# Performance work log

Hardware: AMD Instinct MI355X
Metric: run time of the kernel (lower is better)

Reference implementation:

```python
import jax, jax.numpy as jnp
import numpy as np

INPUT_DIM = 1024
OUTPUT_DIM = 1024
DEGREE = 8
N_TOKENS = 8192


def setup_inputs() -> dict:
    key = jax.random.key(0)
    k1, k2 = jax.random.split(key)
    x = jax.random.normal(k1, (N_TOKENS, INPUT_DIM), dtype=jnp.float32)
    # xavier_normal_ with gain = 1/(input_dim*(degree+1)) over fan dims (output_dim, degree+1)
    fan_in, fan_out = OUTPUT_DIM, DEGREE + 1  # torch treats dim0/dim1 as fans; scale is tiny anyway
    gain = 1.0 / (INPUT_DIM * (DEGREE + 1))
    std = gain * np.sqrt(2.0 / (INPUT_DIM + OUTPUT_DIM))
    cheby_coeffs = std * jax.random.normal(k2, (INPUT_DIM, OUTPUT_DIM, DEGREE + 1), dtype=jnp.float32)
    return {"x": x, "cheby_coeffs": cheby_coeffs}


def reference(x, cheby_coeffs):
    # x: (..., input_dim) -> y: (..., output_dim)
    degree_p1 = cheby_coeffs.shape[-1]
    theta = jnp.arccos(jnp.tanh(x))                      # (..., i)
    arange = jnp.arange(degree_p1, dtype=x.dtype)        # (d,)
    basis = jnp.cos(theta[..., None] * arange)           # (..., i, d) Chebyshev T_d(tanh(x))
    y = jnp.einsum('...id,iod->...o', basis, cheby_coeffs)
    return y
```

## Files before the change

### kernel.cpp

```cpp
#include <hip/hip_runtime.h>


typedef __bf16 bf16;
typedef __bf16 bf16x8 __attribute__((ext_vector_type(8)));
typedef float f32x2 __attribute__((ext_vector_type(2)));
typedef float f32x4 __attribute__((ext_vector_type(4)));
typedef float f32x16 __attribute__((ext_vector_type(16)));

__device__ __forceinline__ void g2lds16(const void* g, void* l) {
  __builtin_amdgcn_global_load_lds(
      (const __attribute__((address_space(1))) unsigned int*)g,
      (__attribute__((address_space(3))) unsigned int*)l, 16, 0, 0);
}

__device__ __forceinline__ float fast_tanh(float a) {
  float e = __expf(a + a);
  return 1.f - 2.f * __builtin_amdgcn_rcpf(e + 1.f);
}

__global__ __launch_bounds__(256)
void cheby_prep(const float* __restrict__ x, const float* __restrict__ C,
                bf16* __restrict__ Bt, float* __restrict__ bias_p,
                float* __restrict__ th) {
  const int bid = blockIdx.x, tid = threadIdx.x;
  if (bid >= 1024) {
    const int r = bid - 1024;
    f32x4 v = *(const f32x4*)(x + (size_t)r * 1024 + tid * 4);
    f32x4 t;
    #pragma unroll
    for (int j = 0; j < 4; ++j) t[j] = fast_tanh(v[j]);
    *(f32x2*)(th + (size_t)r * 1024 + tid * 2)       = (f32x2){t.x, t.z};
    *(f32x2*)(th + (size_t)r * 1024 + 512 + tid * 2) = (f32x2){t.y, t.w};
    return;
  }
  __shared__ float tile[32][292];
  const int i0 = (bid >> 5) * 32, o0 = (bid & 31) * 32;
  {
    const int r = tid >> 3, seg = tid & 7;
    const float* src = C + (size_t)(i0 + r) * 9216 + (size_t)o0 * 9 + seg * 36;
    float* dst = &tile[r][seg * 36];
    #pragma unroll
    for (int v = 0; v < 9; ++v) *(f32x4*)(dst + v * 4) = *(const f32x4*)(src + v * 4);
  }
  __syncthreads();
  #pragma unroll
  for (int j = 0; j < 4; ++j) {
    int e = tid + 256 * j;
    int il = e >> 5, ol = e & 31;
    int i = i0 + il, o = o0 + ol;
    bf16x8 v;
    #pragma unroll
    for (int d = 0; d < 8; ++d) v[d] = (bf16)tile[il][ol * 9 + 1 + d];
    size_t idx16 = ((size_t)((o >> 7) * 128 + (i >> 3)) * 8 + (i & 7)) * 128 + (o & 127);
    *(bf16x8*)&Bt[idx16 * 8] = v;
  }
  if (tid < 32) {
    float s = 0.f;
    #pragma unroll
    for (int i = 0; i < 32; ++i) s += tile[i][tid * 9];
    bias_p[(size_t)(bid >> 5) * 1024 + o0 + tid] = s;
  }
}

__global__ __launch_bounds__(256, 2)
void cheby_gemm(const float* __restrict__ th, const bf16* __restrict__ Bt,
                const float* __restrict__ bias_p, float* __restrict__ out) {
  __shared__ bf16 Bs[2][8192];

  const int tid  = threadIdx.x;
  const int lane = tid & 63, w = tid >> 6;
  const int wm = w >> 1, wn = w & 1;
  const int nb = blockIdx.x & 7, mb = blockIdx.x >> 3;
  const int t0 = mb * 128, o0 = nb * 128;
  const int ml = lane & 31, h = lane >> 5;

  const float* xr0 = th + (size_t)(t0 + wm * 64 + ml) * 1024 + h * 512;
  const float* xr1 = xr0 + 32 * 1024;
  const bf16* btw = Bt + ((size_t)nb * 128 * 1024 + (size_t)w * 256 + lane) * 8;

  f32x16 acc[2][2];
  #pragma unroll
  for (int a = 0; a < 2; ++a)
    #pragma unroll
    for (int b = 0; b < 2; ++b)
      #pragma unroll
      for (int r = 0; r < 16; ++r) acc[a][b][r] = 0.f;

  bf16x8 afrA[2][4], afrB[2][4];
  f32x4 xv0, xv1;

  auto gen = [&](bf16x8 (&dst)[2][4], f32x4 s0, f32x4 s1) {
    #pragma unroll
    for (int ks = 0; ks < 4; ++ks) {
      f32x2 t  = {s0[ks], s1[ks]};
      f32x2 t2 = t + t;
      f32x2 prev = {1.f, 1.f}, cur = t;
      #pragma unroll
      for (int j = 0; j < 8; ++j) {
        dst[0][ks][j] = (bf16)cur.x;
        dst[1][ks][j] = (bf16)cur.y;
        f32x2 nx = t2 * cur - prev;
        prev = cur; cur = nx;
      }
    }
  };

  {
    f32x4 s0 = *(const f32x4*)(xr0), s1 = *(const f32x4*)(xr1);
    gen(afrA, s0, s1);
    xv0 = *(const f32x4*)(xr0 + 4);
    xv1 = *(const f32x4*)(xr1 + 4);
  }
  #pragma unroll
  for (int b = 0; b < 4; ++b)
    g2lds16(btw + (size_t)b * 64 * 8, &Bs[0][(w * 256 + b * 64) * 8]);

  auto stage = [&](int s, int bi, bf16x8 (&cur)[2][4], bf16x8 (&nxt)[2][4]) {
    __syncthreads();
    if (s < 127) {
      const bf16* g = btw + (size_t)(s + 1) * 8192;
      #pragma unroll
      for (int b = 0; b < 4; ++b)
        g2lds16(g + (size_t)b * 64 * 8, &Bs[bi ^ 1][(w * 256 + b * 64) * 8]);
    }
    bf16x8 bfr[4][2];
    #pragma unroll
    for (int ks = 0; ks < 4; ++ks) {
      const int ce = ((ks * 2 + h) * 128 + wn * 64 + ml) * 8;
      bfr[ks][0] = *(const bf16x8*)&Bs[bi][ce];
      bfr[ks][1] = *(const bf16x8*)&Bs[bi][ce + 32 * 8];
    }
    if (s < 127) {
      gen(nxt, xv0, xv1);
      if (s < 126) {
        xv0 = *(const f32x4*)(xr0 + (s + 2) * 4);
        xv1 = *(const f32x4*)(xr1 + (s + 2) * 4);
      }
    }
    #pragma unroll
    for (int ks = 0; ks < 4; ++ks) {
      acc[0][0] = __builtin_amdgcn_mfma_f32_32x32x16_bf16(cur[0][ks], bfr[ks][0], acc[0][0], 0, 0, 0);
      acc[0][1] = __builtin_amdgcn_mfma_f32_32x32x16_bf16(cur[0][ks], bfr[ks][1], acc[0][1], 0, 0, 0);
      acc[1][0] = __builtin_amdgcn_mfma_f32_32x32x16_bf16(cur[1][ks], bfr[ks][0], acc[1][0], 0, 0, 0);
      acc[1][1] = __builtin_amdgcn_mfma_f32_32x32x16_bf16(cur[1][ks], bfr[ks][1], acc[1][1], 0, 0, 0);
    }
  };

  #pragma unroll 1
  for (int s2 = 0; s2 < 64; ++s2) {
    stage(2 * s2,     0, afrA, afrB);
    stage(2 * s2 + 1, 1, afrB, afrA);
  }

  const int c0 = o0 + wn * 64 + ml;
  float bv0 = 0.f, bv1 = 0.f;
  #pragma unroll
  for (int p = 0; p < 32; ++p) {
    bv0 += bias_p[(size_t)p * 1024 + c0];
    bv1 += bias_p[(size_t)p * 1024 + c0 + 32];
  }
  #pragma unroll
  for (int mt = 0; mt < 2; ++mt)
    #pragma unroll
    for (int r = 0; r < 16; ++r) {
      int row = t0 + wm * 64 + mt * 32 + (r & 3) + 8 * (r >> 2) + 4 * h;
      float* po = out + (size_t)row * 1024 + c0;
      po[0]  = acc[mt][0][r] + bv0;
      po[32] = acc[mt][1][r] + bv1;
    }
}

__global__ __launch_bounds__(256)
void cheby_naive(const float* __restrict__ x, const float* __restrict__ C,
                 float* __restrict__ out) {
  const int t = blockIdx.x, tid = threadIdx.x;
  float acc[4] = {0.f, 0.f, 0.f, 0.f};
  for (int i = 0; i < 1024; ++i) {
    float th = tanhf(x[(size_t)t * 1024 + i]);
    float T[9]; T[0] = 1.f; T[1] = th;
    #pragma unroll
    for (int d = 2; d < 9; ++d) T[d] = 2.f * th * T[d - 1] - T[d - 2];
    #pragma unroll
    for (int j = 0; j < 4; ++j) {
      const float* cp = &C[((size_t)i * 1024 + tid + j * 256) * 9];
      float s = 0.f;
      #pragma unroll
      for (int d = 0; d < 9; ++d) s += T[d] * cp[d];
      acc[j] += s;
    }
  }
  #pragma unroll
  for (int j = 0; j < 4; ++j) out[(size_t)t * 1024 + tid + j * 256] = acc[j];
}

extern "C" void kernel_launch(void* const* d_in, const int* in_sizes, int n_in,
                              void* d_out, int out_size, void* d_ws, size_t ws_size,
                              hipStream_t stream) {
  (void)in_sizes; (void)n_in; (void)out_size;
  const float* x = (const float*)d_in[0];
  const float* C = (const float*)d_in[1];
  float* out = (float*)d_out;

  const size_t bt_bytes = (size_t)8 * 128 * 1024 * 8 * sizeof(bf16);
  const size_t bp_bytes = (size_t)32 * 1024 * sizeof(float);
  const size_t th_bytes = (size_t)8192 * 1024 * sizeof(float);

  if (ws_size >= bt_bytes + bp_bytes + th_bytes) {
    bf16*  Bt     = (bf16*)d_ws;
    float* bias_p = (float*)((char*)d_ws + bt_bytes);
    float* th     = (float*)((char*)d_ws + bt_bytes + bp_bytes);
    cheby_prep<<<9216, 256, 0, stream>>>(x, C, Bt, bias_p, th);
    cheby_gemm<<<512, 256, 0, stream>>>(th, Bt, bias_p, out);
  } else {
    cheby_naive<<<8192, 256, 0, stream>>>(x, C, out);
  }
}
```

Before: 269.2 us.

## Split GEMM K dimension in two with atomic accumulation into zeroed output

```diff
diff --git a/kernel.cpp b/kernel.cpp
--- a/kernel.cpp
+++ b/kernel.cpp
@@ -21,7 +21,7 @@
 __global__ __launch_bounds__(256)
 void cheby_prep(const float* __restrict__ x, const float* __restrict__ C,
                 bf16* __restrict__ Bt, float* __restrict__ bias_p,
-                float* __restrict__ th) {
+                float* __restrict__ th, float* __restrict__ out) {
   const int bid = blockIdx.x, tid = threadIdx.x;
   if (bid >= 1024) {
     const int r = bid - 1024;
@@ -31,6 +31,7 @@
     for (int j = 0; j < 4; ++j) t[j] = fast_tanh(v[j]);
     *(f32x2*)(th + (size_t)r * 1024 + tid * 2)       = (f32x2){t.x, t.z};
     *(f32x2*)(th + (size_t)r * 1024 + 512 + tid * 2) = (f32x2){t.y, t.w};
+    *(f32x4*)(out + (size_t)r * 1024 + tid * 4) = (f32x4){0.f, 0.f, 0.f, 0.f};
     return;
   }
   __shared__ float tile[32][292];
@@ -62,7 +63,7 @@
   }
 }
 
-__global__ __launch_bounds__(256, 2)
+__global__ __launch_bounds__(256, 4)
 void cheby_gemm(const float* __restrict__ th, const bf16* __restrict__ Bt,
                 const float* __restrict__ bias_p, float* __restrict__ out) {
   __shared__ bf16 Bs[2][8192];
@@ -70,7 +71,9 @@
   const int tid  = threadIdx.x;
   const int lane = tid & 63, w = tid >> 6;
   const int wm = w >> 1, wn = w & 1;
-  const int nb = blockIdx.x & 7, mb = blockIdx.x >> 3;
+  const int nb = blockIdx.x & 7;
+  const int kh = (blockIdx.x >> 3) & 1;
+  const int mb = blockIdx.x >> 4;
   const int t0 = mb * 128, o0 = nb * 128;
   const int ml = lane & 31, h = lane >> 5;
 
@@ -78,6 +81,8 @@
   const float* xr1 = xr0 + 32 * 1024;
   const bf16* btw = Bt + ((size_t)nb * 128 * 1024 + (size_t)w * 256 + lane) * 8;
 
+  const int sbeg = kh * 64, send = sbeg + 64;
+
   f32x16 acc[2][2];
   #pragma unroll
   for (int a = 0; a < 2; ++a)
@@ -86,78 +91,66 @@
       #pragma unroll
       for (int r = 0; r < 16; ++r) acc[a][b][r] = 0.f;
 
-  bf16x8 afrA[2][4], afrB[2][4];
-  f32x4 xv0, xv1;
-
-  auto gen = [&](bf16x8 (&dst)[2][4], f32x4 s0, f32x4 s1) {
+  f32x4 xv0 = *(const f32x4*)(xr0 + sbeg * 4);
+  f32x4 xv1 = *(const f32x4*)(xr1 + sbeg * 4);
+
+  #pragma unroll
+  for (int b = 0; b < 4; ++b)
+    g2lds16(btw + (size_t)sbeg * 8192 + (size_t)b * 64 * 8,
+            &Bs[0][(w * 256 + b * 64) * 8]);
+
+  #pragma unroll 1
+  for (int s = sbeg; s < send; ++s) {
+    const int bi = (s - sbeg) & 1;
+    __syncthreads();
+    if (s < send - 1) {
+      const bf16* g = btw + (size_t)(s + 1) * 8192;
+      #pragma unroll
+      for (int b = 0; b < 4; ++b)
+        g2lds16(g + (size_t)b * 64 * 8, &Bs[bi ^ 1][(w * 256 + b * 64) * 8]);
+    }
+
+    f32x4 sd0 = xv0, sd1 = xv1;
+    if (s < send - 1) {
+      xv0 = *(const f32x4*)(xr0 + (s + 1) * 4);
+      xv1 = *(const f32x4*)(xr1 + (s + 1) * 4);
+    }
+
+    bf16x8 afr[2][4];
     #pragma unroll
     for (int ks = 0; ks < 4; ++ks) {
-      f32x2 t  = {s0[ks], s1[ks]};
+      f32x2 t  = {sd0[ks], sd1[ks]};
       f32x2 t2 = t + t;
       f32x2 prev = {1.f, 1.f}, cur = t;
       #pragma unroll
       for (int j = 0; j < 8; ++j) {
-        dst[0][ks][j] = (bf16)cur.x;
-        dst[1][ks][j] = (bf16)cur.y;
+        afr[0][ks][j] = (bf16)cur.x;
+        afr[1][ks][j] = (bf16)cur.y;
         f32x2 nx = t2 * cur - prev;
         prev = cur; cur = nx;
       }
     }
-  };
-
-  {
-    f32x4 s0 = *(const f32x4*)(xr0), s1 = *(const f32x4*)(xr1);
-    gen(afrA, s0, s1);
-    xv0 = *(const f32x4*)(xr0 + 4);
-    xv1 = *(const f32x4*)(xr1 + 4);
-  }
-  #pragma unroll
-  for (int b = 0; b < 4; ++b)
-    g2lds16(btw + (size_t)b * 64 * 8, &Bs[0][(w * 256 + b * 64) * 8]);
-
-  auto stage = [&](int s, int bi, bf16x8 (&cur)[2][4], bf16x8 (&nxt)[2][4]) {
-    __syncthreads();
-    if (s < 127) {
-      const bf16* g = btw + (size_t)(s + 1) * 8192;
-      #pragma unroll
-      for (int b = 0; b < 4; ++b)
-        g2lds16(g + (size_t)b * 64 * 8, &Bs[bi ^ 1][(w * 256 + b * 64) * 8]);
-    }
-    bf16x8 bfr[4][2];
+
     #pragma unroll
     for (int ks = 0; ks < 4; ++ks) {
       const int ce = ((ks * 2 + h) * 128 + wn * 64 + ml) * 8;
-      bfr[ks][0] = *(const bf16x8*)&Bs[bi][ce];
-      bfr[ks][1] = *(const bf16x8*)&Bs[bi][ce + 32 * 8];
-    }
-    if (s < 127) {
-      gen(nxt, xv0, xv1);
-      if (s < 126) {
-        xv0 = *(const f32x4*)(xr0 + (s + 2) * 4);
-        xv1 = *(const f32x4*)(xr1 + (s + 2) * 4);
-      }
-    }
-    #pragma unroll
-    for (int ks = 0; ks < 4; ++ks) {
-      acc[0][0] = __builtin_amdgcn_mfma_f32_32x32x16_bf16(cur[0][ks], bfr[ks][0], acc[0][0], 0, 0, 0);
-      acc[0][1] = __builtin_amdgcn_mfma_f32_32x32x16_bf16(cur[0][ks], bfr[ks][1], acc[0][1], 0, 0, 0);
-      acc[1][0] = __builtin_amdgcn_mfma_f32_32x32x16_bf16(cur[1][ks], bfr[ks][0], acc[1][0], 0, 0, 0);
-      acc[1][1] = __builtin_amdgcn_mfma_f32_32x32x16_bf16(cur[1][ks], bfr[ks][1], acc[1][1], 0, 0, 0);
-    }
-  };
-
-  #pragma unroll 1
-  for (int s2 = 0; s2 < 64; ++s2) {
-    stage(2 * s2,     0, afrA, afrB);
-    stage(2 * s2 + 1, 1, afrB, afrA);
+      bf16x8 b0 = *(const bf16x8*)&Bs[bi][ce];
+      bf16x8 b1 = *(const bf16x8*)&Bs[bi][ce + 32 * 8];
+      acc[0][0] = __builtin_amdgcn_mfma_f32_32x32x16_bf16(afr[0][ks], b0, acc[0][0], 0, 0, 0);
+      acc[0][1] = __builtin_amdgcn_mfma_f32_32x32x16_bf16(afr[0][ks], b1, acc[0][1], 0, 0, 0);
+      acc[1][0] = __builtin_amdgcn_mfma_f32_32x32x16_bf16(afr[1][ks], b0, acc[1][0], 0, 0, 0);
+      acc[1][1] = __builtin_amdgcn_mfma_f32_32x32x16_bf16(afr[1][ks], b1, acc[1][1], 0, 0, 0);
+    }
   }
 
   const int c0 = o0 + wn * 64 + ml;
   float bv0 = 0.f, bv1 = 0.f;
-  #pragma unroll
-  for (int p = 0; p < 32; ++p) {
-    bv0 += bias_p[(size_t)p * 1024 + c0];
-    bv1 += bias_p[(size_t)p * 1024 + c0 + 32];
+  if (kh == 0) {
+    #pragma unroll
+    for (int p = 0; p < 32; ++p) {
+      bv0 += bias_p[(size_t)p * 1024 + c0];
+      bv1 += bias_p[(size_t)p * 1024 + c0 + 32];
+    }
   }
   #pragma unroll
   for (int mt = 0; mt < 2; ++mt)
@@ -165,8 +158,8 @@
     for (int r = 0; r < 16; ++r) {
       int row = t0 + wm * 64 + mt * 32 + (r & 3) + 8 * (r >> 2) + 4 * h;
       float* po = out + (size_t)row * 1024 + c0;
-      po[0]  = acc[mt][0][r] + bv0;
-      po[32] = acc[mt][1][r] + bv1;
+      unsafeAtomicAdd(&po[0],  acc[mt][0][r] + bv0);
+      unsafeAtomicAdd(&po[32], acc[mt][1][r] + bv1);
     }
 }
 
@@ -209,8 +202,8 @@
     bf16*  Bt     = (bf16*)d_ws;
     float* bias_p = (float*)((char*)d_ws + bt_bytes);
     float* th     = (float*)((char*)d_ws + bt_bytes + bp_bytes);
-    cheby_prep<<<9216, 256, 0, stream>>>(x, C, Bt, bias_p, th);
-    cheby_gemm<<<512, 256, 0, stream>>>(th, Bt, bias_p, out);
+    cheby_prep<<<9216, 256, 0, stream>>>(x, C, Bt, bias_p, th, out);
+    cheby_gemm<<<1024, 256, 0, stream>>>(th, Bt, bias_p, out);
   } else {
     cheby_naive<<<8192, 256, 0, stream>>>(x, C, out);
   }
```

New measurement: 299.3 us. 1.11x slower.

## Load B fragments directly from global into registers, dropping LDS staging and barriers

Applied to the files above, without the earlier changes.

```diff
diff --git a/kernel.cpp b/kernel.cpp
--- a/kernel.cpp
+++ b/kernel.cpp
@@ -6,12 +6,6 @@
 typedef float f32x2 __attribute__((ext_vector_type(2)));
 typedef float f32x4 __attribute__((ext_vector_type(4)));
 typedef float f32x16 __attribute__((ext_vector_type(16)));
-
-__device__ __forceinline__ void g2lds16(const void* g, void* l) {
-  __builtin_amdgcn_global_load_lds(
-      (const __attribute__((address_space(1))) unsigned int*)g,
-      (__attribute__((address_space(3))) unsigned int*)l, 16, 0, 0);
-}
 
 __device__ __forceinline__ float fast_tanh(float a) {
   float e = __expf(a + a);
@@ -65,18 +59,18 @@
 __global__ __launch_bounds__(256, 2)
 void cheby_gemm(const float* __restrict__ th, const bf16* __restrict__ Bt,
                 const float* __restrict__ bias_p, float* __restrict__ out) {
-  __shared__ bf16 Bs[2][8192];
-
   const int tid  = threadIdx.x;
   const int lane = tid & 63, w = tid >> 6;
-  const int wm = w >> 1, wn = w & 1;
-  const int nb = blockIdx.x & 7, mb = blockIdx.x >> 3;
-  const int t0 = mb * 128, o0 = nb * 128;
   const int ml = lane & 31, h = lane >> 5;
-
-  const float* xr0 = th + (size_t)(t0 + wm * 64 + ml) * 1024 + h * 512;
-  const float* xr1 = xr0 + 32 * 1024;
-  const bf16* btw = Bt + ((size_t)nb * 128 * 1024 + (size_t)w * 256 + lane) * 8;
+  const int nb = blockIdx.x & 7;
+  const int mb = blockIdx.x >> 3;
+  const int wn = w & 1, wm = w >> 1;
+  const int t0 = mb * 128 + wm * 64;
+  const int o0 = nb * 128 + wn * 64;
+
+  const bf16* btl = Bt + (((size_t)nb * 1024 + h) * 128 + (size_t)wn * 64 + ml) * 8;
+  const float* sp0 = th + (size_t)(t0 + ml) * 1024 + h * 512;
+  const float* sp1 = sp0 + 32 * 1024;
 
   f32x16 acc[2][2];
   #pragma unroll
@@ -86,85 +80,79 @@
       #pragma unroll
       for (int r = 0; r < 16; ++r) acc[a][b][r] = 0.f;
 
-  bf16x8 afrA[2][4], afrB[2][4];
-  f32x4 xv0, xv1;
-
-  auto gen = [&](bf16x8 (&dst)[2][4], f32x4 s0, f32x4 s1) {
-    #pragma unroll
-    for (int ks = 0; ks < 4; ++ks) {
-      f32x2 t  = {s0[ks], s1[ks]};
-      f32x2 t2 = t + t;
-      f32x2 prev = {1.f, 1.f}, cur = t;
-      #pragma unroll
-      for (int j = 0; j < 8; ++j) {
-        dst[0][ks][j] = (bf16)cur.x;
-        dst[1][ks][j] = (bf16)cur.y;
-        f32x2 nx = t2 * cur - prev;
-        prev = cur; cur = nx;
+  f32x4  sa[4], sb[4];
+  bf16x8 bfr[2][4][2];
+
+  sa[0] = *(const f32x4*)(sp0);     sb[0] = *(const f32x4*)(sp1);
+  sa[1] = *(const f32x4*)(sp0 + 4); sb[1] = *(const f32x4*)(sp1 + 4);
+  #pragma unroll
+  for (int ks = 0; ks < 4; ++ks) {
+    bfr[0][ks][0] = *(const bf16x8*)(btl + ks * 2048);
+    bfr[0][ks][1] = *(const bf16x8*)(btl + ks * 2048 + 256);
+  }
+
+  #pragma unroll 1
+  for (int s4 = 0; s4 < 128; s4 += 4) {
+    #pragma unroll
+    for (int u = 0; u < 4; ++u) {
+      const int s = s4 + u;
+      {
+        int sl = s + 2; if (sl > 127) sl = 127;
+        sa[(u + 2) & 3] = *(const f32x4*)(sp0 + sl * 4);
+        sb[(u + 2) & 3] = *(const f32x4*)(sp1 + sl * 4);
+      }
+      {
+        int bl = s + 1; if (bl > 127) bl = 127;
+        const bf16* g = btl + (size_t)bl * 8192;
+        #pragma unroll
+        for (int ks = 0; ks < 4; ++ks) {
+          bfr[(u + 1) & 1][ks][0] = *(const bf16x8*)(g + ks * 2048);
+          bfr[(u + 1) & 1][ks][1] = *(const bf16x8*)(g + ks * 2048 + 256);
+        }
+      }
+      bf16x8 afr[2][4];
+      #pragma unroll
+      for (int r = 0; r < 2; ++r) {
+        const f32x4 sd = r ? sb[u & 3] : sa[u & 3];
+        #pragma unroll
+        for (int ks = 0; ks < 4; ++ks) {
+          const float t  = sd[ks];
+          const float T2 = __builtin_fmaf(t + t, t, -1.f);
+          const float c2 = T2 + T2;
+          const f32x2 c2v = {c2, c2};
+          f32x2 pm1 = {t, 1.f};
+          f32x2 p   = {t, T2};
+          #pragma unroll
+          for (int j2 = 0; j2 < 4; ++j2) {
+            afr[r][ks][2 * j2]     = (bf16)p.x;
+            afr[r][ks][2 * j2 + 1] = (bf16)p.y;
+            f32x2 pn = c2v * p - pm1;
+            pm1 = p; p = pn;
+          }
+        }
+      }
+      #pragma unroll
+      for (int ks = 0; ks < 4; ++ks) {
+        acc[0][0] = __builtin_amdgcn_mfma_f32_32x32x16_bf16(afr[0][ks], bfr[u & 1][ks][0], acc[0][0], 0, 0, 0);
+        acc[0][1] = __builtin_amdgcn_mfma_f32_32x32x16_bf16(afr[0][ks], bfr[u & 1][ks][1], acc[0][1], 0, 0, 0);
+        acc[1][0] = __builtin_amdgcn_mfma_f32_32x32x16_bf16(afr[1][ks], bfr[u & 1][ks][0], acc[1][0], 0, 0, 0);
+        acc[1][1] = __builtin_amdgcn_mfma_f32_32x32x16_bf16(afr[1][ks], bfr[u & 1][ks][1], acc[1][1], 0, 0, 0);
       }
     }
-  };
-
-  {
-    f32x4 s0 = *(const f32x4*)(xr0), s1 = *(const f32x4*)(xr1);
-    gen(afrA, s0, s1);
-    xv0 = *(const f32x4*)(xr0 + 4);
-    xv1 = *(const f32x4*)(xr1 + 4);
-  }
-  #pragma unroll
-  for (int b = 0; b < 4; ++b)
-    g2lds16(btw + (size_t)b * 64 * 8, &Bs[0][(w * 256 + b * 64) * 8]);
-
-  auto stage = [&](int s, int bi, bf16x8 (&cur)[2][4], bf16x8 (&nxt)[2][4]) {
-    __syncthreads();
-    if (s < 127) {
-      const bf16* g = btw + (size_t)(s + 1) * 8192;
-      #pragma unroll
-      for (int b = 0; b < 4; ++b)
-        g2lds16(g + (size_t)b * 64 * 8, &Bs[bi ^ 1][(w * 256 + b * 64) * 8]);
-    }
-    bf16x8 bfr[4][2];
-    #pragma unroll
-    for (int ks = 0; ks < 4; ++ks) {
-      const int ce = ((ks * 2 + h) * 128 + wn * 64 + ml) * 8;
-      bfr[ks][0] = *(const bf16x8*)&Bs[bi][ce];
-      bfr[ks][1] = *(const bf16x8*)&Bs[bi][ce + 32 * 8];
-    }
-    if (s < 127) {
-      gen(nxt, xv0, xv1);
-      if (s < 126) {
-        xv0 = *(const f32x4*)(xr0 + (s + 2) * 4);
-        xv1 = *(const f32x4*)(xr1 + (s + 2) * 4);
-      }
-    }
-    #pragma unroll
-    for (int ks = 0; ks < 4; ++ks) {
-      acc[0][0] = __builtin_amdgcn_mfma_f32_32x32x16_bf16(cur[0][ks], bfr[ks][0], acc[0][0], 0, 0, 0);
-      acc[0][1] = __builtin_amdgcn_mfma_f32_32x32x16_bf16(cur[0][ks], bfr[ks][1], acc[0][1], 0, 0, 0);
-      acc[1][0] = __builtin_amdgcn_mfma_f32_32x32x16_bf16(cur[1][ks], bfr[ks][0], acc[1][0], 0, 0, 0);
-      acc[1][1] = __builtin_amdgcn_mfma_f32_32x32x16_bf16(cur[1][ks], bfr[ks][1], acc[1][1], 0, 0, 0);
-    }
-  };
-
-  #pragma unroll 1
-  for (int s2 = 0; s2 < 64; ++s2) {
-    stage(2 * s2,     0, afrA, afrB);
-    stage(2 * s2 + 1, 1, afrB, afrA);
-  }
-
-  const int c0 = o0 + wn * 64 + ml;
+  }
+
   float bv0 = 0.f, bv1 = 0.f;
   #pragma unroll
   for (int p = 0; p < 32; ++p) {
-    bv0 += bias_p[(size_t)p * 1024 + c0];
-    bv1 += bias_p[(size_t)p * 1024 + c0 + 32];
+    bv0 += bias_p[(size_t)p * 1024 + o0 + ml];
+    bv1 += bias_p[(size_t)p * 1024 + o0 + 32 + ml];
   }
   #pragma unroll
   for (int mt = 0; mt < 2; ++mt)
     #pragma unroll
     for (int r = 0; r < 16; ++r) {
-      int row = t0 + wm * 64 + mt * 32 + (r & 3) + 8 * (r >> 2) + 4 * h;
-      float* po = out + (size_t)row * 1024 + c0;
+      int row = t0 + mt * 32 + (r & 3) + 8 * (r >> 2) + 4 * h;
+      float* po = out + (size_t)row * 1024 + o0 + ml;
       po[0]  = acc[mt][0][r] + bv0;
       po[32] = acc[mt][1][r] + bv1;
     }
```

After: 290.2 us. 7.8% more time.
